# Kernel tuning notes

Measured on AMD Instinct MI355X. Metric: run time of the kernel, lower is better.

The kernel has to match this reference:

```python
import jax, jax.numpy as jnp
import numpy as np

DIM, HEADS, RANK = 768, 12, 64
HEAD_DIM = DIM // HEADS

def _xavier(key, shape):
    fan_in, fan_out = shape[1], shape[0]
    std = (2.0 / (fan_in + fan_out)) ** 0.5
    return std * jax.random.normal(key, shape, dtype=jnp.float32)

def setup_inputs() -> dict:
    key = jax.random.key(0)
    ks = jax.random.split(key, 12)
    B, N = 8, 1024
    x = jax.random.normal(ks[0], (B, N, DIM), dtype=jnp.float32)
    params = {}
    for i, nm in enumerate(['Q', 'K', 'V']):
        params[f'W_{nm}0'] = _xavier(ks[1 + 3 * i], (DIM, RANK))
        params[f'W_{nm}1'] = _xavier(ks[2 + 3 * i], (HEADS, RANK))
        params[f'W_{nm}2'] = _xavier(ks[3 + 3 * i], (HEAD_DIM, RANK))
    proj_w = _xavier(ks[10], (DIM, DIM))
    proj_b = jnp.zeros((DIM,), dtype=jnp.float32)
    return dict(x=x, W_Q0=params['W_Q0'], W_Q1=params['W_Q1'], W_Q2=params['W_Q2'],
                W_K0=params['W_K0'], W_K1=params['W_K1'], W_K2=params['W_K2'],
                W_V0=params['W_V0'], W_V1=params['W_V1'], W_V2=params['W_V2'],
                proj_w=proj_w, proj_b=proj_b)

def _cp_proj(xh, W2, W1, W0, B, N, H, hd):
    # xh: [B,N,H,hd]; contract head_dim with W2 and heads with W1 -> [B,N,R], then expand to dim via W0
    t = jnp.einsum('blnd,dr,nr->blr', xh, W2, W1)
    out = jnp.einsum('blr,mr->blm', t, W0)          # [B,N,dim]
    return out.reshape(B, N, H, hd).transpose(0, 2, 1, 3)  # [B,H,N,hd]

def reference(x, W_Q0, W_Q1, W_Q2, W_K0, W_K1, W_K2, W_V0, W_V1, W_V2, proj_w, proj_b):
    B, N, C = x.shape
    H = W_Q1.shape[0]
    hd = C // H
    scale = hd ** -0.5
    xh = x.reshape(B, N, H, hd)
    q = _cp_proj(xh, W_Q2, W_Q1, W_Q0, B, N, H, hd)
    k = _cp_proj(xh, W_K2, W_K1, W_K0, B, N, H, hd)
    v = _cp_proj(xh, W_V2, W_V1, W_V0, B, N, H, hd)
    attn = jax.nn.softmax(jnp.einsum('bhqd,bhkd->bhqk', q, k) * scale, axis=-1)
    out = jnp.einsum('bhqk,bhkd->bhqd', attn, v).transpose(0, 2, 1, 3).reshape(B, N, C)
    return out @ proj_w.T + proj_b
```

## Files before the change

### kernel.cpp

```cpp
#include <hip/hip_runtime.h>

typedef unsigned short u16;
typedef __attribute__((ext_vector_type(8))) short bf16x8;
typedef __attribute__((ext_vector_type(4))) float f32x4;
typedef __attribute__((ext_vector_type(4))) unsigned short u16x4;
typedef __attribute__((ext_vector_type(8))) unsigned short u16x8;

#define AS1 __attribute__((address_space(1)))
#define AS3 __attribute__((address_space(3)))

__device__ __forceinline__ u16 f2b(float f) {
    unsigned u = __float_as_uint(f);
    unsigned r = 0x7fffu + ((u >> 16) & 1u);
    return (u16)((u + r) >> 16);
}

__device__ __forceinline__ unsigned packtrunc(float p0, float p1) {
#if __has_builtin(__builtin_amdgcn_perm)
    return __builtin_amdgcn_perm(__float_as_uint(p1), __float_as_uint(p0), 0x07060302u);
#else
    return (__float_as_uint(p0) >> 16) | (__float_as_uint(p1) & 0xffff0000u);
#endif
}

__device__ __forceinline__ void g2l16(const u16* g, u16* l) {
    __builtin_amdgcn_global_load_lds((const AS1 void*)g, (AS3 void*)l, 16, 0, 0);
}

#if __has_builtin(__builtin_amdgcn_exp2f)
#define EXP2(x) __builtin_amdgcn_exp2f(x)
#else
#define EXP2(x) exp2f(x)
#endif

__device__ unsigned g_cnt[2];
__device__ unsigned g_gen[2];

__device__ __forceinline__ void gbar(int i, unsigned nblk) {
    __syncthreads();
    if (threadIdx.x == 0) {
        __threadfence();
        const unsigned my = __hip_atomic_load(&g_gen[i], __ATOMIC_RELAXED,
                                              __HIP_MEMORY_SCOPE_AGENT);
        const unsigned v = __hip_atomic_fetch_add(&g_cnt[i], 1u, __ATOMIC_ACQ_REL,
                                                  __HIP_MEMORY_SCOPE_AGENT);
        if (v == nblk - 1u) {
            __hip_atomic_store(&g_cnt[i], 0u, __ATOMIC_RELAXED,
                               __HIP_MEMORY_SCOPE_AGENT);
            __threadfence();
            __hip_atomic_fetch_add(&g_gen[i], 1u, __ATOMIC_ACQ_REL,
                                   __HIP_MEMORY_SCOPE_AGENT);
        } else {
            unsigned spins = 0;
            while (__hip_atomic_load(&g_gen[i], __ATOMIC_ACQUIRE,
                                     __HIP_MEMORY_SCOPE_AGENT) == my) {
                __builtin_amdgcn_s_sleep(2);
                if (++spins > (1u << 22)) break;
            }
        }
        __threadfence();
    }
    __syncthreads();
}

__device__ __forceinline__ void phaseA(
    const int bid, const int t, char* smem,
    const float* __restrict__ X,
    const float* __restrict__ Wq0, const float* __restrict__ Wq1, const float* __restrict__ Wq2,
    const float* __restrict__ Wk0, const float* __restrict__ Wk1, const float* __restrict__ Wk2,
    const float* __restrict__ Wv0, const float* __restrict__ Wv1, const float* __restrict__ Wv2,
    const float* __restrict__ PW,
    u16* __restrict__ T, u16* __restrict__ tvt,
    u16* __restrict__ MqkT, u16* __restrict__ Dcat)
{
    const f32x4 zero4 = {0.f, 0.f, 0.f, 0.f};
    if (bid < 384) {
        u16*   As  = (u16*)smem;
        u16*   Bs  = (u16*)(smem + 4096);
        float* W1t = (float*)(smem + 8192);
        float* W2t = (float*)(smem + 11264);

        const int lane = t & 63, wv = t >> 6;
        const int l15 = lane & 15, quad = lane >> 4;

        const int lin = bid;
        const int xcd = lin & 7, j = lin >> 3;
        const int col = j % 3, rowhi = j / 3;
        const int rowBase = (rowhi * 8 + xcd) * 64;
        const int colBase = col * 64;

        const float* W1g = (col == 0) ? Wq1 : (col == 1) ? Wk1 : Wv1;
        const float* W2g = (col == 0) ? Wq2 : (col == 1) ? Wk2 : Wv2;
        for (int i = t; i < 768; i += 256) W1t[i] = W1g[i];
        for (int i = t; i < 4096; i += 256) {
            const int d = i >> 6, r = i & 63;
            W2t[r * 65 + d] = W2g[i];
        }

        const int srow = t >> 2;
        const int scol = (t & 3) * 8;
        const float* aS = X + (size_t)(rowBase + srow) * 768 + scol;

        float4 a0 = *(const float4*)(aS);
        float4 a1 = *(const float4*)(aS + 4);

        f32x4 acc[4];
#pragma unroll
        for (int tn = 0; tn < 4; ++tn) acc[tn] = zero4;

        for (int kk = 0; kk < 768; kk += 32) {
            __syncthreads();
            u16x8 ap;
            ap[0] = f2b(a0.x); ap[1] = f2b(a0.y); ap[2] = f2b(a0.z); ap[3] = f2b(a0.w);
            ap[4] = f2b(a1.x); ap[5] = f2b(a1.y); ap[6] = f2b(a1.z); ap[7] = f2b(a1.w);
            *(u16x8*)&As[srow * 32 + scol] = ap;
            {
                const int c0 = kk + scol;
                const int hh = c0 >> 6, dd = c0 & 63;
                const float w1v = W1t[hh * 64 + srow];
                u16x8 bp;
#pragma unroll
                for (int jj = 0; jj < 8; ++jj)
                    bp[jj] = f2b(w1v * W2t[srow * 65 + dd + jj]);
                *(u16x8*)&Bs[srow * 32 + scol] = bp;
            }
            __syncthreads();

            if (kk < 736) {
                a0 = *(const float4*)(aS + kk + 32);
                a1 = *(const float4*)(aS + kk + 36);
            }

            const bf16x8 af = *(const bf16x8*)(As + (wv * 16 + l15) * 32 + quad * 8);
#pragma unroll
            for (int tn = 0; tn < 4; ++tn) {
                const bf16x8 bf = *(const bf16x8*)(Bs + (tn * 16 + l15) * 32 + quad * 8);
                acc[tn] = __builtin_amdgcn_mfma_f32_16x16x32_bf16(af, bf, acc[tn], 0, 0, 0);
            }
        }

        if (colBase < 128) {
#pragma unroll
            for (int tn = 0; tn < 4; ++tn) {
                const int c = colBase + tn * 16 + l15;
#pragma unroll
                for (int r = 0; r < 4; ++r) {
                    const int grow = rowBase + wv * 16 + quad * 4 + r;
                    T[(size_t)grow * 128 + c] = f2b(acc[tn][r]);
                }
            }
        } else {
#pragma unroll
            for (int tn = 0; tn < 4; ++tn) {
                const int rr = tn * 16 + l15;
                const int grow = rowBase + wv * 16 + quad * 4;
                u16x4 pk;
                pk.x = f2b(acc[tn][0]); pk.y = f2b(acc[tn][1]);
                pk.z = f2b(acc[tn][2]); pk.w = f2b(acc[tn][3]);
                *(u16x4*)(tvt + (size_t)rr * 8192 + grow) = pk;
            }
        }
    } else if (bid < 432) {
        float* wq = (float*)smem;
        float* wk = (float*)(smem + 16640);
        const int hq = bid - 384;
        const int h = hq >> 2, quarter = hq & 3;
        const float qs = 0.125f * 1.4426950408889634f;
        for (int i = t; i < 4096; i += 256) {
            const int dd = i >> 6, r = i & 63;
            wq[dd * 65 + r] = Wq0[(h * 64 + dd) * 64 + r] * qs;
            wk[dd * 65 + r] = Wk0[(h * 64 + dd) * 64 + r];
        }
        __syncthreads();
        const int j0 = quarter * 1024 + t * 4;
        const int r2 = j0 >> 6, r1b = j0 & 63;
        u16x4 pk;
#pragma unroll
        for (int jj = 0; jj < 4; ++jj) {
            float acc = 0.f;
#pragma unroll
            for (int dd = 0; dd < 64; ++dd)
                acc += wk[dd * 65 + r2] * wq[dd * 65 + r1b + jj];
            ((u16*)&pk)[jj] = f2b(acc);
        }
        *(u16x4*)(MqkT + (size_t)(h * 64 + r2) * 64 + r1b) = pk;
    } else if (bid < 720) {
        float* w0s = (float*)smem;
        float* pws = (float*)(smem + 16640);
        const int hb = bid - 432;
        const int h = hb / 24, mBase = (hb - h * 24) * 32;
        for (int i = t; i < 4096; i += 256) {
            const int d = i >> 6, r = i & 63;
            w0s[d * 65 + r] = Wv0[(h * 64 + d) * 64 + r];
        }
        for (int i = t; i < 2048; i += 256) {
            const int mi = i >> 6, d = i & 63;
            pws[mi * 65 + d] = PW[(size_t)(mBase + mi) * 768 + h * 64 + d];
        }
        __syncthreads();
        const int r = t & 63, mi0 = t >> 6;
        float w0c[64];
#pragma unroll
        for (int d = 0; d < 64; ++d) w0c[d] = w0s[d * 65 + r];
        for (int mi = mi0; mi < 32; mi += 4) {
            float acc = 0.f;
#pragma unroll
            for (int d = 0; d < 64; ++d) acc += pws[mi * 65 + d] * w0c[d];
            Dcat[(size_t)(mBase + mi) * 768 + h * 64 + r] = f2b(acc);
        }
    }
}

__device__ __forceinline__ void phaseB(
    const int bid, const int t, char* smem,
    const u16* __restrict__ T, const u16* __restrict__ MqkT,
    const u16* __restrict__ tvt, u16* __restrict__ Zcat)
{
    const int bh = bid % 96;
    const int qt = bid / 96;
    const int b = bh / 12, h = bh - b * 12;
    const u16* qp = T + ((size_t)b * 1024 + qt * 128) * 128;
    const u16* kp = T + (size_t)b * 1024 * 128 + 64;
    const u16* vp = tvt + b * 1024;

    u16* const B0raw = (u16*)smem;
    u16* const B1raw = (u16*)(smem + 18432);

    const int lane = t & 63, wv = t >> 6;
    const int l15 = lane & 15, quad = lane >> 4;
    const f32x4 zero4 = {0.f, 0.f, 0.f, 0.f};

    bf16x8 qf[2][2];
#pragma unroll
    for (int qg = 0; qg < 2; ++qg) {
        const u16* qrow = qp + (size_t)(wv * 32 + qg * 16 + l15) * 128;
        qf[qg][0] = *(const bf16x8*)(qrow + quad * 8);
        qf[qg][1] = *(const bf16x8*)(qrow + 32 + quad * 8);
    }

    const int srow = t >> 2;
    const int scol = (t & 3) * 16;
    const int p5 = srow & 31;
    const int lrow = (srow & 32) | ((p5 & 4) << 2) | ((p5 & 16) >> 1)
                   | ((p5 & 8) >> 1) | (p5 & 3);

    bf16x8 vone = {};
    if (l15 == 0) {
#pragma unroll
        for (int j = 0; j < 8; ++j) vone[j] = (short)0x3F80;
    }

    int4 kr0 = *(const int4*)(kp + (size_t)srow * 128 + scol);
    int4 kr1 = *(const int4*)(kp + (size_t)srow * 128 + scol + 8);
    int4 vr0 = *(const int4*)(vp + (size_t)srow * 8192 + scol);
    int4 vr1 = *(const int4*)(vp + (size_t)srow * 8192 + scol + 8);

    {
        f32x4 Wt[2][4];
#pragma unroll
        for (int qg = 0; qg < 2; ++qg)
#pragma unroll
            for (int tn = 0; tn < 4; ++tn) Wt[qg][tn] = zero4;
#pragma unroll
        for (int ks = 0; ks < 2; ++ks) {
#pragma unroll
            for (int tn = 0; tn < 4; ++tn) {
                const bf16x8 mb = *(const bf16x8*)(
                    MqkT + (size_t)(h * 64 + tn * 16 + l15) * 64 + ks * 32 + quad * 8);
                Wt[0][tn] = __builtin_amdgcn_mfma_f32_16x16x32_bf16(qf[0][ks], mb, Wt[0][tn], 0, 0, 0);
                Wt[1][tn] = __builtin_amdgcn_mfma_f32_16x16x32_bf16(qf[1][ks], mb, Wt[1][tn], 0, 0, 0);
            }
        }
#pragma unroll
        for (int qg = 0; qg < 2; ++qg)
#pragma unroll
            for (int tn = 0; tn < 4; ++tn)
#pragma unroll
                for (int r = 0; r < 4; ++r)
                    B1raw[(wv * 32 + qg * 16 + quad * 4 + r) * 72 + tn * 16 + l15] =
                        f2b(Wt[qg][tn][r]);
    }
    __syncthreads();
    bf16x8 wf[2][2];
#pragma unroll
    for (int qg = 0; qg < 2; ++qg) {
        wf[qg][0] = *(const bf16x8*)&B1raw[(wv * 32 + qg * 16 + l15) * 72 + quad * 8];
        wf[qg][1] = *(const bf16x8*)&B1raw[(wv * 32 + qg * 16 + l15) * 72 + 32 + quad * 8];
    }

    *(int4*)&B0raw[lrow * 72 + scol]                 = kr0;
    *(int4*)&B0raw[lrow * 72 + scol + 8]             = kr1;
    *(int4*)&B0raw[64 * 72 + srow * 72 + scol]       = vr0;
    *(int4*)&B0raw[64 * 72 + srow * 72 + scol + 8]   = vr1;
    kr0 = *(const int4*)(kp + (size_t)(64 + srow) * 128 + scol);
    kr1 = *(const int4*)(kp + (size_t)(64 + srow) * 128 + scol + 8);
    vr0 = *(const int4*)(vp + (size_t)srow * 8192 + 64 + scol);
    vr1 = *(const int4*)(vp + (size_t)srow * 8192 + 64 + scol + 8);
    __syncthreads();

    f32x4 o_acc[2][4];
    f32x4 Lacc[2] = {zero4, zero4};
#pragma unroll
    for (int qg = 0; qg < 2; ++qg)
#pragma unroll
        for (int tn = 0; tn < 4; ++tn) o_acc[qg][tn] = zero4;

#define STAGE(NB)                                                               \
    {                                                                           \
        *(int4*)&NB[lrow * 72 + scol]               = kr0;                      \
        *(int4*)&NB[lrow * 72 + scol + 8]           = kr1;                      \
        *(int4*)&NB[64 * 72 + srow * 72 + scol]     = vr0;                      \
        *(int4*)&NB[64 * 72 + srow * 72 + scol + 8] = vr1;                      \
    }
#define PREFETCH(KT)                                                            \
    {                                                                           \
        kr0 = *(const int4*)(kp + (size_t)((KT) * 64 + srow) * 128 + scol);     \
        kr1 = *(const int4*)(kp + (size_t)((KT) * 64 + srow) * 128 + scol + 8); \
        vr0 = *(const int4*)(vp + (size_t)srow * 8192 + (KT) * 64 + scol);      \
        vr1 = *(const int4*)(vp + (size_t)srow * 8192 + (KT) * 64 + scol + 8);  \
    }
#define FLASH_TILE(KB)                                                          \
    {                                                                           \
        f32x4 Sacc[2][4];                                                       \
        _Pragma("unroll")                                                       \
        for (int qg = 0; qg < 2; ++qg)                                          \
            _Pragma("unroll")                                                   \
            for (int tk = 0; tk < 4; ++tk) Sacc[qg][tk] = zero4;                \
        _Pragma("unroll")                                                       \
        for (int ks = 0; ks < 2; ++ks) {                                        \
            _Pragma("unroll")                                                   \
            for (int tk = 0; tk < 4; ++tk) {                                    \
                const bf16x8 kf = *(const bf16x8*)&KB[(tk * 16 + l15) * 72 + ks * 32 + quad * 8]; \
                Sacc[0][tk] = __builtin_amdgcn_mfma_f32_16x16x32_bf16(kf, wf[0][ks], Sacc[0][tk], 0, 0, 0); \
                Sacc[1][tk] = __builtin_amdgcn_mfma_f32_16x16x32_bf16(kf, wf[1][ks], Sacc[1][tk], 0, 0, 0); \
            }                                                                   \
        }                                                                       \
        union { bf16x8 v; unsigned u[4]; } pf[2][2];                            \
        _Pragma("unroll")                                                       \
        for (int qg = 0; qg < 2; ++qg)                                          \
            _Pragma("unroll")                                                   \
            for (int tk = 0; tk < 4; ++tk) {                                    \
                const float p0 = EXP2(Sacc[qg][tk][0]);                         \
                const float p1 = EXP2(Sacc[qg][tk][1]);                         \
                const float p2 = EXP2(Sacc[qg][tk][2]);                         \
                const float p3 = EXP2(Sacc[qg][tk][3]);                         \
                const int g = tk >> 1, hf = (tk & 1) * 2;                       \
                pf[qg][g].u[hf + 0] = packtrunc(p0, p1);                        \
                pf[qg][g].u[hf + 1] = packtrunc(p2, p3);                        \
            }                                                                   \
        _Pragma("unroll")                                                       \
        for (int g = 0; g < 2; ++g) {                                           \
            _Pragma("unroll")                                                   \
            for (int tn = 0; tn < 4; ++tn) {                                    \
                const bf16x8 vf = *(const bf16x8*)&KB[64 * 72 + (tn * 16 + l15) * 72 + g * 32 + quad * 8]; \
                o_acc[0][tn] = __builtin_amdgcn_mfma_f32_16x16x32_bf16(pf[0][g].v, vf, o_acc[0][tn], 0, 0, 0); \
                o_acc[1][tn] = __builtin_amdgcn_mfma_f32_16x16x32_bf16(pf[1][g].v, vf, o_acc[1][tn], 0, 0, 0); \
            }                                                                   \
            Lacc[0] = __builtin_amdgcn_mfma_f32_16x16x32_bf16(pf[0][g].v, vone, Lacc[0], 0, 0, 0); \
            Lacc[1] = __builtin_amdgcn_mfma_f32_16x16x32_bf16(pf[1][g].v, vone, Lacc[1], 0, 0, 0); \
        }                                                                       \
    }

    for (int t8 = 0; t8 < 8; ++t8) {
        const int kt0 = 2 * t8;
        STAGE(B1raw);
        if (t8 < 7) PREFETCH(kt0 + 2);
        FLASH_TILE(B0raw);
        __syncthreads();
        if (t8 < 7) {
            STAGE(B0raw);
            PREFETCH(kt0 + 3);
        }
        FLASH_TILE(B1raw);
        if (t8 < 7) __syncthreads();
    }

#undef STAGE
#undef PREFETCH
#undef FLASH_TILE

#pragma unroll
    for (int qg = 0; qg < 2; ++qg) {
#pragma unroll
        for (int r = 0; r < 4; ++r) {
            const float Lv = __shfl(Lacc[qg][r], quad << 4, 64);
            const float inv = 1.0f / Lv;
            const int token = qt * 128 + wv * 32 + qg * 16 + quad * 4 + r;
#pragma unroll
            for (int tn = 0; tn < 4; ++tn) {
                const int col = h * 64 + tn * 16 + l15;
                Zcat[(size_t)(b * 1024 + token) * 768 + col] = f2b(o_acc[qg][tn][r] * inv);
            }
        }
    }
}

__device__ __forceinline__ void phaseC(
    const int bid, const int t, char* smem,
    const u16* __restrict__ Zcat, const u16* __restrict__ Dcat,
    float* __restrict__ outp, const float* __restrict__ bias)
{
    u16* As = (u16*)smem;
    u16* Bs = (u16*)(smem + 8192);

    const int lane = t & 63, wv = t >> 6;
    const int l15 = lane & 15, quad = lane >> 4;
    const f32x4 zero4 = {0.f, 0.f, 0.f, 0.f};

    const int lin = bid;
    const int xcd = lin & 7, j = lin >> 3;
    const int colT = j % 12, rowhi = j / 12;
    const int rowBase = (rowhi * 8 + xcd) * 128;
    const int colBase = colT * 64;

    const int srowA = wv * 32 + (lane >> 2);
    const int srowB = wv * 16 + (lane >> 2);
    const int scol  = (lane & 3) * 8;
    const u16* aSrc = Zcat + (size_t)(rowBase + srowA) * 768 + scol;
    const u16* bSrc = Dcat + (size_t)(colBase + srowB) * 768 + scol;
    u16* aDst = As + wv * 1024;
    u16* bDst = Bs + wv * 512;

    f32x4 acc[2][4];
#pragma unroll
    for (int tm = 0; tm < 2; ++tm)
#pragma unroll
        for (int tn = 0; tn < 4; ++tn) acc[tm][tn] = zero4;

    for (int kk = 0; kk < 768; kk += 32) {
        __syncthreads();
        g2l16(aSrc + kk,            aDst);
        g2l16(aSrc + kk + 16 * 768, aDst + 512);
        g2l16(bSrc + kk,            bDst);
        __syncthreads();

        bf16x8 af[2], bfm[4];
#pragma unroll
        for (int tt = 0; tt < 2; ++tt)
            af[tt]  = *(const bf16x8*)(As + (wv * 32 + tt * 16 + l15) * 32 + quad * 8);
#pragma unroll
        for (int tt = 0; tt < 4; ++tt)
            bfm[tt] = *(const bf16x8*)(Bs + (tt * 16 + l15) * 32 + quad * 8);
#pragma unroll
        for (int tm = 0; tm < 2; ++tm)
#pragma unroll
            for (int tn = 0; tn < 4; ++tn)
                acc[tm][tn] = __builtin_amdgcn_mfma_f32_16x16x32_bf16(
                    af[tm], bfm[tn], acc[tm][tn], 0, 0, 0);
    }

#pragma unroll
    for (int tm = 0; tm < 2; ++tm) {
        const int grow = rowBase + wv * 32 + tm * 16 + quad * 4;
#pragma unroll
        for (int tn = 0; tn < 4; ++tn) {
            const int gcol = colBase + tn * 16 + l15;
            const float bv = bias[gcol];
#pragma unroll
            for (int r = 0; r < 4; ++r)
                outp[(size_t)(grow + r) * 768 + gcol] = acc[tm][tn][r] + bv;
        }
    }
}

__global__ __launch_bounds__(256, 3) void mega(
    const float* __restrict__ X,
    const float* __restrict__ Wq0, const float* __restrict__ Wq1, const float* __restrict__ Wq2,
    const float* __restrict__ Wk0, const float* __restrict__ Wk1, const float* __restrict__ Wk2,
    const float* __restrict__ Wv0, const float* __restrict__ Wv1, const float* __restrict__ Wv2,
    const float* __restrict__ PW, const float* __restrict__ bias,
    u16* __restrict__ T, u16* __restrict__ tvt,
    u16* __restrict__ MqkT, u16* __restrict__ Dcat,
    u16* __restrict__ Zcat, float* __restrict__ outp)
{
    __shared__ __align__(16) char smem[36864];
    const int bid = blockIdx.x, t = threadIdx.x;
    if (bid < 720)
        phaseA(bid, t, smem, X, Wq0, Wq1, Wq2, Wk0, Wk1, Wk2, Wv0, Wv1, Wv2, PW,
               T, tvt, MqkT, Dcat);
    gbar(0, 768u);
    phaseB(bid, t, smem, T, MqkT, tvt, Zcat);
    gbar(1, 768u);
    phaseC(bid, t, smem, Zcat, Dcat, outp, bias);
}

__global__ __launch_bounds__(256, 2) void k_prep(
    const float* __restrict__ X,
    const float* __restrict__ Wq0, const float* __restrict__ Wq1, const float* __restrict__ Wq2,
    const float* __restrict__ Wk0, const float* __restrict__ Wk1, const float* __restrict__ Wk2,
    const float* __restrict__ Wv0, const float* __restrict__ Wv1, const float* __restrict__ Wv2,
    const float* __restrict__ PW,
    u16* __restrict__ T, u16* __restrict__ tvt,
    u16* __restrict__ MqkT, u16* __restrict__ Dcat)
{
    __shared__ __align__(16) char smem[36864];
    phaseA(blockIdx.x, threadIdx.x, smem, X, Wq0, Wq1, Wq2, Wk0, Wk1, Wk2,
           Wv0, Wv1, Wv2, PW, T, tvt, MqkT, Dcat);
}

__global__ __launch_bounds__(256, 3) void k_flash(
    const u16* __restrict__ T, const u16* __restrict__ MqkT,
    const u16* __restrict__ tvt, u16* __restrict__ Zcat)
{
    __shared__ __align__(16) char smem[36864];
    phaseB(blockIdx.x + 96 * blockIdx.y, threadIdx.x, smem, T, MqkT, tvt, Zcat);
}

__global__ __launch_bounds__(256, 3) void k_out(
    const u16* __restrict__ Zcat, const u16* __restrict__ Dcat,
    float* __restrict__ outp, const float* __restrict__ bias)
{
    __shared__ __align__(16) char smem[36864];
    phaseC(blockIdx.x, threadIdx.x, smem, Zcat, Dcat, outp, bias);
}

extern "C" void kernel_launch(void* const* d_in, const int* in_sizes, int n_in,
                              void* d_out, int out_size, void* d_ws, size_t ws_size,
                              hipStream_t stream)
{
    const float* x      = (const float*)d_in[0];
    const float* Wq0    = (const float*)d_in[1];
    const float* Wq1    = (const float*)d_in[2];
    const float* Wq2    = (const float*)d_in[3];
    const float* Wk0    = (const float*)d_in[4];
    const float* Wk1    = (const float*)d_in[5];
    const float* Wk2    = (const float*)d_in[6];
    const float* Wv0    = (const float*)d_in[7];
    const float* Wv1    = (const float*)d_in[8];
    const float* Wv2    = (const float*)d_in[9];
    const float* proj_w = (const float*)d_in[10];
    const float* proj_b = (const float*)d_in[11];
    float* outp = (float*)d_out;

    char* ws = (char*)d_ws;
    u16* T    = (u16*)ws;
    u16* tvt  = (u16*)(ws + 2097152);
    u16* MqkT = (u16*)(ws + 3440640);
    u16* Dcat = (u16*)(ws + 3538944);
    u16* Zcat = (u16*)(ws + 4718592);

    static int use_mega = -1;
    if (use_mega < 0) {
        int nb = 0;
        hipError_t e = hipOccupancyMaxActiveBlocksPerMultiprocessor(&nb, mega, 256, 0);
        use_mega = (e == hipSuccess && nb >= 3) ? 1 : 0;
    }

    if (use_mega) {
        mega<<<768, 256, 0, stream>>>(x, Wq0, Wq1, Wq2, Wk0, Wk1, Wk2,
                                      Wv0, Wv1, Wv2, proj_w, proj_b,
                                      T, tvt, MqkT, Dcat, Zcat, outp);
    } else {
        k_prep<<<720, 256, 0, stream>>>(x, Wq0, Wq1, Wq2, Wk0, Wk1, Wk2,
                                        Wv0, Wv1, Wv2, proj_w,
                                        T, tvt, MqkT, Dcat);
        k_flash<<<dim3(96, 8), 256, 0, stream>>>(T, MqkT, tvt, Zcat);
        k_out<<<768, 256, 0, stream>>>(Zcat, Dcat, outp, proj_b);
    }
}
```

Measured before the change: 165.3 us.

## Widen K-step to 64 with XOR-swizzled LDS tiles and register prefetch

```diff
diff --git a/kernel.cpp b/kernel.cpp
--- a/kernel.cpp
+++ b/kernel.cpp
@@ -21,10 +21,6 @@
 #else
     return (__float_as_uint(p0) >> 16) | (__float_as_uint(p1) & 0xffff0000u);
 #endif
-}
-
-__device__ __forceinline__ void g2l16(const u16* g, u16* l) {
-    __builtin_amdgcn_global_load_lds((const AS1 void*)g, (AS3 void*)l, 16, 0, 0);
 }
 
 #if __has_builtin(__builtin_amdgcn_exp2f)
@@ -76,9 +72,9 @@
     const f32x4 zero4 = {0.f, 0.f, 0.f, 0.f};
     if (bid < 384) {
         u16*   As  = (u16*)smem;
-        u16*   Bs  = (u16*)(smem + 4096);
-        float* W1t = (float*)(smem + 8192);
-        float* W2t = (float*)(smem + 11264);
+        u16*   Bs  = (u16*)(smem + 8192);
+        float* W1t = (float*)(smem + 16384);
+        float* W2t = (float*)(smem + 19456);
 
         const int lane = t & 63, wv = t >> 6;
         const int l15 = lane & 15, quad = lane >> 4;
@@ -98,44 +94,65 @@
         }
 
         const int srow = t >> 2;
-        const int scol = (t & 3) * 8;
+        const int sc4  = t & 3;
+        const int scol = sc4 * 16;
+        const int swa = ((sc4 * 2)     ^ (srow & 7)) * 8;
+        const int swb = ((sc4 * 2 + 1) ^ (srow & 7)) * 8;
         const float* aS = X + (size_t)(rowBase + srow) * 768 + scol;
 
         float4 a0 = *(const float4*)(aS);
         float4 a1 = *(const float4*)(aS + 4);
+        float4 a2 = *(const float4*)(aS + 8);
+        float4 a3 = *(const float4*)(aS + 12);
 
         f32x4 acc[4];
 #pragma unroll
         for (int tn = 0; tn < 4; ++tn) acc[tn] = zero4;
 
-        for (int kk = 0; kk < 768; kk += 32) {
+        for (int kk = 0; kk < 768; kk += 64) {
             __syncthreads();
-            u16x8 ap;
-            ap[0] = f2b(a0.x); ap[1] = f2b(a0.y); ap[2] = f2b(a0.z); ap[3] = f2b(a0.w);
-            ap[4] = f2b(a1.x); ap[5] = f2b(a1.y); ap[6] = f2b(a1.z); ap[7] = f2b(a1.w);
-            *(u16x8*)&As[srow * 32 + scol] = ap;
+            u16x8 ap0, ap1;
+            ap0[0] = f2b(a0.x); ap0[1] = f2b(a0.y); ap0[2] = f2b(a0.z); ap0[3] = f2b(a0.w);
+            ap0[4] = f2b(a1.x); ap0[5] = f2b(a1.y); ap0[6] = f2b(a1.z); ap0[7] = f2b(a1.w);
+            ap1[0] = f2b(a2.x); ap1[1] = f2b(a2.y); ap1[2] = f2b(a2.z); ap1[3] = f2b(a2.w);
+            ap1[4] = f2b(a3.x); ap1[5] = f2b(a3.y); ap1[6] = f2b(a3.z); ap1[7] = f2b(a3.w);
+            *(u16x8*)&As[srow * 64 + swa] = ap0;
+            *(u16x8*)&As[srow * 64 + swb] = ap1;
             {
                 const int c0 = kk + scol;
                 const int hh = c0 >> 6, dd = c0 & 63;
                 const float w1v = W1t[hh * 64 + srow];
-                u16x8 bp;
+                u16x8 bp0, bp1;
 #pragma unroll
                 for (int jj = 0; jj < 8; ++jj)
-                    bp[jj] = f2b(w1v * W2t[srow * 65 + dd + jj]);
-                *(u16x8*)&Bs[srow * 32 + scol] = bp;
+                    bp0[jj] = f2b(w1v * W2t[srow * 65 + dd + jj]);
+#pragma unroll
+                for (int jj = 0; jj < 8; ++jj)
+                    bp1[jj] = f2b(w1v * W2t[srow * 65 + dd + 8 + jj]);
+                *(u16x8*)&Bs[srow * 64 + swa] = bp0;
+                *(u16x8*)&Bs[srow * 64 + swb] = bp1;
             }
             __syncthreads();
 
-            if (kk < 736) {
-                a0 = *(const float4*)(aS + kk + 32);
-                a1 = *(const float4*)(aS + kk + 36);
-            }
-
-            const bf16x8 af = *(const bf16x8*)(As + (wv * 16 + l15) * 32 + quad * 8);
-#pragma unroll
-            for (int tn = 0; tn < 4; ++tn) {
-                const bf16x8 bf = *(const bf16x8*)(Bs + (tn * 16 + l15) * 32 + quad * 8);
-                acc[tn] = __builtin_amdgcn_mfma_f32_16x16x32_bf16(af, bf, acc[tn], 0, 0, 0);
+            if (kk < 704) {
+                a0 = *(const float4*)(aS + kk + 64);
+                a1 = *(const float4*)(aS + kk + 68);
+                a2 = *(const float4*)(aS + kk + 72);
+                a3 = *(const float4*)(aS + kk + 76);
+            }
+
+            const int arow = wv * 16 + l15;
+#pragma unroll
+            for (int ks = 0; ks < 2; ++ks) {
+                const bf16x8 af = *(const bf16x8*)
+                    &As[arow * 64 + ((ks * 4 + quad) ^ (arow & 7)) * 8];
+#pragma unroll
+                for (int tn = 0; tn < 4; ++tn) {
+                    const int brow = tn * 16 + l15;
+                    const bf16x8 bf = *(const bf16x8*)
+                        &Bs[brow * 64 + ((ks * 4 + quad) ^ (brow & 7)) * 8];
+                    acc[tn] = __builtin_amdgcn_mfma_f32_16x16x32_bf16(af, bf, acc[tn], 0, 0, 0);
+                }
             }
         }
 
@@ -401,7 +418,7 @@
     float* __restrict__ outp, const float* __restrict__ bias)
 {
     u16* As = (u16*)smem;
-    u16* Bs = (u16*)(smem + 8192);
+    u16* Bs = (u16*)(smem + 16384);
 
     const int lane = t & 63, wv = t >> 6;
     const int l15 = lane & 15, quad = lane >> 4;
@@ -415,11 +432,21 @@
 
     const int srowA = wv * 32 + (lane >> 2);
     const int srowB = wv * 16 + (lane >> 2);
-    const int scol  = (lane & 3) * 8;
+    const int sc4   = lane & 3;
+    const int scol  = sc4 * 16;
+    const int swa0 = ((sc4 * 2)     ^ (srowA & 7)) * 8;
+    const int swa1 = ((sc4 * 2 + 1) ^ (srowA & 7)) * 8;
+    const int swb0 = ((sc4 * 2)     ^ (srowB & 7)) * 8;
+    const int swb1 = ((sc4 * 2 + 1) ^ (srowB & 7)) * 8;
     const u16* aSrc = Zcat + (size_t)(rowBase + srowA) * 768 + scol;
     const u16* bSrc = Dcat + (size_t)(colBase + srowB) * 768 + scol;
-    u16* aDst = As + wv * 1024;
-    u16* bDst = Bs + wv * 512;
+
+    int4 ar0 = *(const int4*)(aSrc);
+    int4 ar1 = *(const int4*)(aSrc + 8);
+    int4 ar2 = *(const int4*)(aSrc + 16 * 768);
+    int4 ar3 = *(const int4*)(aSrc + 16 * 768 + 8);
+    int4 br0 = *(const int4*)(bSrc);
+    int4 br1 = *(const int4*)(bSrc + 8);
 
     f32x4 acc[2][4];
 #pragma unroll
@@ -427,26 +454,47 @@
 #pragma unroll
         for (int tn = 0; tn < 4; ++tn) acc[tm][tn] = zero4;
 
-    for (int kk = 0; kk < 768; kk += 32) {
+    for (int kk = 0; kk < 768; kk += 64) {
         __syncthreads();
-        g2l16(aSrc + kk,            aDst);
-        g2l16(aSrc + kk + 16 * 768, aDst + 512);
-        g2l16(bSrc + kk,            bDst);
+        *(int4*)&As[srowA * 64 + swa0]        = ar0;
+        *(int4*)&As[srowA * 64 + swa1]        = ar1;
+        *(int4*)&As[(srowA + 16) * 64 + swa0] = ar2;
+        *(int4*)&As[(srowA + 16) * 64 + swa1] = ar3;
+        *(int4*)&Bs[srowB * 64 + swb0]        = br0;
+        *(int4*)&Bs[srowB * 64 + swb1]        = br1;
         __syncthreads();
 
-        bf16x8 af[2], bfm[4];
-#pragma unroll
-        for (int tt = 0; tt < 2; ++tt)
-            af[tt]  = *(const bf16x8*)(As + (wv * 32 + tt * 16 + l15) * 32 + quad * 8);
-#pragma unroll
-        for (int tt = 0; tt < 4; ++tt)
-            bfm[tt] = *(const bf16x8*)(Bs + (tt * 16 + l15) * 32 + quad * 8);
-#pragma unroll
-        for (int tm = 0; tm < 2; ++tm)
-#pragma unroll
-            for (int tn = 0; tn < 4; ++tn)
-                acc[tm][tn] = __builtin_amdgcn_mfma_f32_16x16x32_bf16(
-                    af[tm], bfm[tn], acc[tm][tn], 0, 0, 0);
+        if (kk < 704) {
+            ar0 = *(const int4*)(aSrc + kk + 64);
+            ar1 = *(const int4*)(aSrc + kk + 72);
+            ar2 = *(const int4*)(aSrc + 16 * 768 + kk + 64);
+            ar3 = *(const int4*)(aSrc + 16 * 768 + kk + 72);
+            br0 = *(const int4*)(bSrc + kk + 64);
+            br1 = *(const int4*)(bSrc + kk + 72);
+        }
+
+#pragma unroll
+        for (int ks = 0; ks < 2; ++ks) {
+            bf16x8 af[2], bfm[4];
+#pragma unroll
+            for (int tm = 0; tm < 2; ++tm) {
+                const int arow = wv * 32 + tm * 16 + l15;
+                af[tm] = *(const bf16x8*)
+                    &As[arow * 64 + ((ks * 4 + quad) ^ (arow & 7)) * 8];
+            }
+#pragma unroll
+            for (int tn = 0; tn < 4; ++tn) {
+                const int brow = tn * 16 + l15;
+                bfm[tn] = *(const bf16x8*)
+                    &Bs[brow * 64 + ((ks * 4 + quad) ^ (brow & 7)) * 8];
+            }
+#pragma unroll
+            for (int tm = 0; tm < 2; ++tm)
+#pragma unroll
+                for (int tn = 0; tn < 4; ++tn)
+                    acc[tm][tn] = __builtin_amdgcn_mfma_f32_16x16x32_bf16(
+                        af[tm], bfm[tn], acc[tm][tn], 0, 0, 0);
+        }
     }
 
 #pragma unroll
```

Measured after the change: 155.2 us, median of 2. -6.1%, faster.
